# Kernel optimization log

Hardware: AMD Instinct MI355X
Metric: run time of the kernel (lower is better)

## Reference

```python
import jax, jax.numpy as jnp
import numpy as np

B, L, D, F = 1, 4096, 4096, 11008
# (start, end, side): side 0 = vision expert, side 1 = language expert.
# Mirrors merge_section_size over alternating contiguous vision/language token ranges.
SEGMENTS = [(0, 1024, 0), (1024, 2048, 1), (2048, 3072, 0), (3072, 4096, 1)]


def setup_inputs() -> dict:
    key = jax.random.key(0)
    ks = jax.random.split(key, 7)
    s = 0.02  # weight init scale
    hidden_states = jax.random.normal(ks[0], (B, L, D), jnp.float32)
    tt = np.zeros((B, L), np.int32)
    for a, b, side in SEGMENTS:
        tt[:, a:b] = side
    token_type_ids = jnp.asarray(tt)
    lg_w = jax.random.normal(ks[1], (D, F), jnp.float32) * s
    lu_w = jax.random.normal(ks[2], (D, F), jnp.float32) * s
    ld_w = jax.random.normal(ks[3], (F, D), jnp.float32) * s
    vg_w = jax.random.normal(ks[4], (D, F), jnp.float32) * s
    vu_w = jax.random.normal(ks[5], (D, F), jnp.float32) * s
    vd_w = jax.random.normal(ks[6], (F, D), jnp.float32) * s
    return {
        'hidden_states': hidden_states,
        'token_type_ids': token_type_ids,
        'lg_w': lg_w, 'lu_w': lu_w, 'ld_w': ld_w,
        'vg_w': vg_w, 'vu_w': vu_w, 'vd_w': vd_w,
    }


def _swiglu_mlp(x, gw, uw, dw):
    # x: [B, T, D] -> [B, T, D]; down(silu(gate(x)) * up(x))
    h = jax.nn.silu(jnp.einsum('btd,df->btf', x, gw)) * jnp.einsum('btd,df->btf', x, uw)
    return jnp.einsum('btf,fd->btd', h, dw)


def reference(hidden_states, token_type_ids, lg_w, lu_w, ld_w, vg_w, vu_w, vd_w):
    # Split-dispatch over static contiguous segments, then concat along seq dim.
    outs = []
    for a, b, side in SEGMENTS:
        seg = hidden_states[:, a:b, :]
        if side == 1:
            outs.append(_swiglu_mlp(seg, lg_w, lu_w, ld_w))
        else:
            outs.append(_swiglu_mlp(seg, vg_w, vu_w, vd_w))
    return jnp.concatenate(outs, axis=1)
```

## Files before the change

kernel.cpp:

```cpp
#include <hip/hip_runtime.h>
#include <math.h>

typedef unsigned short u16;
typedef short s16x8 __attribute__((ext_vector_type(8)));
typedef float f32x4 __attribute__((ext_vector_type(4)));

#define GLOAD16(gp, lp)                                                        \
  __builtin_amdgcn_global_load_lds(                                            \
      (const __attribute__((address_space(1))) void*)(gp),                     \
      (__attribute__((address_space(3))) void*)(lp), 16, 0, 0)

__device__ __forceinline__ u16 f2bf(float f) {
  union { float f; unsigned u; } v; v.f = f;
  unsigned r = v.u + 0x7fffu + ((v.u >> 16) & 1u);
  return (u16)(r >> 16);
}

__global__ __launch_bounds__(256) void prep_kernel(
    const float* __restrict__ in0, const float* __restrict__ in1,
    const float* __restrict__ in2, const float* __restrict__ in3,
    const float* __restrict__ in4, const float* __restrict__ in5,
    const float* __restrict__ xin,
    u16* __restrict__ o01, u16* __restrict__ o23,
    u16* __restrict__ o4, u16* __restrict__ o5, u16* __restrict__ xout) {
  const int mat = blockIdx.y;
  const int t = threadIdx.x;
  if (mat == 6) {
    if (blockIdx.x >= 8192) return;
    size_t i = ((size_t)blockIdx.x * 256 + t) * 8;
    float4 a = *(const float4*)(xin + i);
    float4 b = *(const float4*)(xin + i + 4);
    s16x8 v;
    v[0] = (short)f2bf(a.x); v[1] = (short)f2bf(a.y);
    v[2] = (short)f2bf(a.z); v[3] = (short)f2bf(a.w);
    v[4] = (short)f2bf(b.x); v[5] = (short)f2bf(b.y);
    v[6] = (short)f2bf(b.z); v[7] = (short)f2bf(b.w);
    *(s16x8*)(xout + i) = v;
    return;
  }
  __shared__ float s[64 * 65];
  const float* in; u16* out;
  switch (mat) {
    case 0: in = in0; out = o01; break;
    case 1: in = in1; out = o01; break;
    case 2: in = in2; out = o23; break;
    case 3: in = in3; out = o23; break;
    case 4: in = in4; out = o4; break;
    default: in = in5; out = o5; break;
  }
  const int R = (mat < 4) ? 4096 : 11008;
  const int C = (mat < 4) ? 11008 : 4096;
  const int nTc = C >> 6;
  const int tr = blockIdx.x / nTc, tc = blockIdx.x - tr * nTc;
  const int r0 = tr << 6, c0 = tc << 6;
#pragma unroll
  for (int p = 0; p < 4; ++p) {
    const int lr = p * 16 + (t >> 4);
    const int lc = (t & 15) * 4;
    float4 v = *(const float4*)(in + (size_t)(r0 + lr) * C + (c0 + lc));
    float* sp = &s[lr * 65 + lc];
    sp[0] = v.x; sp[1] = v.y; sp[2] = v.z; sp[3] = v.w;
  }
  __syncthreads();
#pragma unroll
  for (int q = 0; q < 2; ++q) {
    const int oc = q * 32 + (t >> 3);
    const int orr = (t & 7) * 8;
    s16x8 v;
#pragma unroll
    for (int i = 0; i < 8; ++i) v[i] = (short)f2bf(s[(orr + i) * 65 + oc]);
    const int f = c0 + oc;
    size_t orow;
    if (mat < 4) orow = (size_t)((f >> 4) << 5) + ((mat & 1) << 4) + (f & 15);
    else         orow = (size_t)f;
    *(s16x8*)(out + orow * R + (r0 + orr)) = v;
  }
}

#define SBAR() __builtin_amdgcn_s_barrier()
#define LGKM0() asm volatile("s_waitcnt lgkmcnt(0)")
#define LGKM8() asm volatile("s_waitcnt lgkmcnt(8)")
#define VMCNT6() asm volatile("s_waitcnt vmcnt(6)")
#define VMCNT0() asm volatile("s_waitcnt vmcnt(0)")

__global__ __launch_bounds__(512, 1) void gemm_gateup_persist(
    const u16* __restrict__ A, const u16* __restrict__ Bl,
    const u16* __restrict__ Bv, const int* __restrict__ tt,
    u16* __restrict__ H) {
  __shared__ u16 sA[2][2][128][64];
  __shared__ u16 sB[2][2][128][64];

  const int bid = blockIdx.x;
  const int c = ((bid >> 7) << 3) | (bid & 7);
  const int mT = (bid >> 3) & 15;
  const int ntiles = (c < 6) ? 6 : 5;
  const int FK = ntiles * 64;

  const int t = threadIdx.x;
  const int lane = t & 63;
  const int rlo = lane & 15;
  const int hi = lane >> 4;
  const int wn = (t >> 6) & 3;
  const int wm = (t >> 8) & 1;

  const int side = tt[mT << 8];
  const u16* B = side ? Bl : Bv;

  const int rowq = t >> 3;
  const int gsw = ((t & 7) ^ (rowq & 7)) << 4;
  const char* srcA = (const char*)A + (size_t)(mT * 256 + rowq) * 8192 + gsw;
  const char* srcB0 = (const char*)B + ((size_t)(c * 256) + rowq) * 8192 + gsw;
  char* ldsA = (char*)&sA[0][0][0][0];
  char* ldsB = (char*)&sB[0][0][0][0];
  const int woff = (t & 448) << 4;

#define PSTG_A(d, h, q)                                                        \
  do {                                                                         \
    const char* _pa = srcA + ((q) & 63) * 128;                                 \
    GLOAD16(_pa + (size_t)((h) * 128) * 8192,                                  \
            ldsA + (d) * 32768 + (h) * 16384 + woff);                          \
    GLOAD16(_pa + (size_t)((h) * 128 + 64) * 8192,                             \
            ldsA + (d) * 32768 + (h) * 16384 + 8192 + woff);                   \
  } while (0)
#define PSTG_B(d, h, q)                                                        \
  do {                                                                         \
    const char* _pb = srcB0 + (size_t)((q) >> 6) * 33554432 +                  \
                      (size_t)((h) * 128) * 8192 + ((q) & 63) * 128;           \
    GLOAD16(_pb, ldsB + (d) * 32768 + (h) * 16384 + woff);                     \
    GLOAD16(_pb + (size_t)64 * 8192,                                           \
            ldsB + (d) * 32768 + (h) * 16384 + 8192 + woff);                   \
  } while (0)

  const int cxa = (hi ^ (rlo & 7)) << 4;
  const int cxb = ((4 + hi) ^ (rlo & 7)) << 4;
  const int arow = (wm * 64 + rlo) * 128;
  const int brow = (wn * 32 + rlo) * 128;

  s16x8 af[4][2], bf[2][2][2];
  f32x4 acc[8][4];
  const f32x4 z = {0.f, 0.f, 0.f, 0.f};
#pragma unroll
  for (int i = 0; i < 8; ++i)
#pragma unroll
    for (int j = 0; j < 4; ++j) acc[i][j] = z;

#define LDA(d, mh)                                                             \
  do {                                                                         \
    _Pragma("unroll") for (int fi = 0; fi < 4; ++fi) {                         \
      const char* p = ldsA + (d) * 32768 + (mh) * 16384 + arow + fi * 2048;    \
      af[fi][0] = *(const s16x8*)(p + cxa);                                    \
      af[fi][1] = *(const s16x8*)(p + cxb);                                    \
    }                                                                          \
  } while (0)
#define LDBS(bi, d, nh)                                                        \
  do {                                                                         \
    _Pragma("unroll") for (int gi = 0; gi < 2; ++gi) {                         \
      const char* p = ldsB + (d) * 32768 + (nh) * 16384 + brow + gi * 2048;    \
      bf[bi][gi][0] = *(const s16x8*)(p + cxa);                                \
      bf[bi][gi][1] = *(const s16x8*)(p + cxb);                                \
    }                                                                          \
  } while (0)
#define MFMA16(mh, nh)                                                         \
  do {                                                                         \
    __builtin_amdgcn_s_setprio(1);                                             \
    _Pragma("unroll") for (int fi = 0; fi < 4; ++fi)                           \
        _Pragma("unroll") for (int gi = 0; gi < 2; ++gi) {                     \
      acc[(mh)*4 + fi][(nh)*2 + gi] = __builtin_amdgcn_mfma_f32_16x16x32_bf16( \
          af[fi][0], bf[nh][gi][0], acc[(mh)*4 + fi][(nh)*2 + gi], 0, 0, 0);   \
      acc[(mh)*4 + fi][(nh)*2 + gi] = __builtin_amdgcn_mfma_f32_16x16x32_bf16( \
          af[fi][1], bf[nh][gi][1], acc[(mh)*4 + fi][(nh)*2 + gi], 0, 0, 0);   \
    }                                                                          \
    __builtin_amdgcn_s_setprio(0);                                             \
  } while (0)

#define GU_EPI(nTv)                                                            \
  do {                                                                         \
    const int _nT = (nTv);                                                     \
    _Pragma("unroll") for (int mh = 0; mh < 2; ++mh)                           \
        _Pragma("unroll") for (int fi = 0; fi < 4; ++fi) {                     \
      const int row0 = mT * 256 + mh * 128 + wm * 64 + fi * 16 + hi * 4;       \
      _Pragma("unroll") for (int nh = 0; nh < 2; ++nh) {                       \
        const int fc = _nT * 128 + (nh * 4 + wn) * 16 + rlo;                   \
        const f32x4 g = acc[mh * 4 + fi][nh * 2 + 0];                          \
        const f32x4 u = acc[mh * 4 + fi][nh * 2 + 1];                          \
        _Pragma("unroll") for (int r = 0; r < 4; ++r) {                        \
          const float gv = g[r];                                               \
          const float hv = gv / (1.f + __expf(-gv)) * u[r];                    \
          H[(size_t)(row0 + r) * 11008 + fc] = f2bf(hv);                       \
        }                                                                      \
      }                                                                        \
    }                                                                          \
  } while (0)

  PSTG_A(0, 0, 0); PSTG_B(0, 0, 0); PSTG_B(0, 1, 0); PSTG_A(0, 1, 0);
  PSTG_A(1, 0, 1); PSTG_B(1, 0, 1); PSTG_B(1, 1, 1);
  VMCNT6();
  SBAR();

  for (int T = 0; T < FK - 2; T += 2) {
    LDA(0, 0); LDBS(0, 0, 0);
    PSTG_A(1, 1, T + 1);
    LGKM8();
    SBAR(); LGKM0(); MFMA16(0, 0); SBAR();
    LDBS(1, 0, 1);
    PSTG_A(0, 0, T + 2);
    SBAR(); LGKM0(); MFMA16(0, 1); SBAR();
    LDA(0, 1);
    PSTG_B(0, 0, T + 2);
    SBAR(); LGKM0(); MFMA16(1, 1); SBAR();
    PSTG_B(0, 1, T + 2);
    VMCNT6();
    SBAR(); MFMA16(1, 0); SBAR();
    LDA(1, 0); LDBS(0, 1, 0);
    PSTG_A(0, 1, T + 2);
    LGKM8();
    SBAR(); LGKM0(); MFMA16(0, 0); SBAR();
    LDBS(1, 1, 1);
    PSTG_A(1, 0, T + 3);
    SBAR(); LGKM0(); MFMA16(0, 1); SBAR();
    LDA(1, 1);
    PSTG_B(1, 0, T + 3);
    SBAR(); LGKM0(); MFMA16(1, 1); SBAR();
    PSTG_B(1, 1, T + 3);
    VMCNT6();
    SBAR(); MFMA16(1, 0); SBAR();

    if ((T & 63) == 62) {
      GU_EPI(c + 16 * (T >> 6));
#pragma unroll
      for (int i = 0; i < 8; ++i)
#pragma unroll
        for (int j = 0; j < 4; ++j) acc[i][j] = z;
    }
  }
  {
    LDA(0, 0); LDBS(0, 0, 0);
    PSTG_A(1, 1, FK - 1);
    LGKM8();
    SBAR(); LGKM0(); MFMA16(0, 0); SBAR();
    LDBS(1, 0, 1);
    SBAR(); LGKM0(); MFMA16(0, 1); SBAR();
    LDA(0, 1);
    SBAR(); LGKM0(); MFMA16(1, 1); SBAR();
    VMCNT0();
    SBAR(); MFMA16(1, 0); SBAR();
    LDA(1, 0); LDBS(0, 1, 0);
    LGKM8();
    SBAR(); LGKM0(); MFMA16(0, 0); SBAR();
    LDBS(1, 1, 1);
    SBAR(); LGKM0(); MFMA16(0, 1); SBAR();
    LDA(1, 1);
    SBAR(); LGKM0(); MFMA16(1, 1); SBAR();
    MFMA16(1, 0);
  }
  GU_EPI(c + 16 * (ntiles - 1));
#undef PSTG_A
#undef PSTG_B
#undef LDA
#undef LDBS
#undef MFMA16
#undef GU_EPI
}

__global__ __launch_bounds__(512, 1) void gemm_down(
    const u16* __restrict__ A, const u16* __restrict__ Bl,
    const u16* __restrict__ Bv, const int* __restrict__ tt,
    float* __restrict__ O) {
  constexpr int KB = 22016;
  constexpr int NK = KB / 128;
  __shared__ u16 sA[2][2][128][64];
  __shared__ u16 sB[2][2][128][64];

  const int bid = blockIdx.x;
  const int wg = (bid & 7) * 32 + (bid >> 3);
  const int mT = wg & 15;
  const int nT = wg >> 4;

  const int t = threadIdx.x;
  const int lane = t & 63;
  const int rlo = lane & 15;
  const int hi = lane >> 4;
  const int wn = (t >> 6) & 3;
  const int wm = (t >> 8) & 1;

  const int side = tt[mT << 8];
  const u16* B = side ? Bl : Bv;

  const int rowq = t >> 3;
  const int gsw = ((t & 7) ^ (rowq & 7)) << 4;
  const char* srcA = (const char*)A + (size_t)(mT * 256 + rowq) * KB + gsw;
  const char* srcB = (const char*)B + (size_t)(nT * 256 + rowq) * KB + gsw;
  char* ldsA = (char*)&sA[0][0][0][0];
  char* ldsB = (char*)&sB[0][0][0][0];
  const int woff = (t & 448) << 4;

#define STG_A(d, h, kt)                                                        \
  do {                                                                         \
    GLOAD16(srcA + (size_t)((h) * 128) * KB + (kt) * 128,                      \
            ldsA + (d) * 32768 + (h) * 16384 + woff);                          \
    GLOAD16(srcA + (size_t)((h) * 128 + 64) * KB + (kt) * 128,                 \
            ldsA + (d) * 32768 + (h) * 16384 + 8192 + woff);                   \
  } while (0)
#define STG_B(d, h, kt)                                                        \
  do {                                                                         \
    GLOAD16(srcB + (size_t)((h) * 128) * KB + (kt) * 128,                      \
            ldsB + (d) * 32768 + (h) * 16384 + woff);                          \
    GLOAD16(srcB + (size_t)((h) * 128 + 64) * KB + (kt) * 128,                 \
            ldsB + (d) * 32768 + (h) * 16384 + 8192 + woff);                   \
  } while (0)

  const int cxa = (hi ^ (rlo & 7)) << 4;
  const int cxb = ((4 + hi) ^ (rlo & 7)) << 4;
  const int arow = (wm * 64 + rlo) * 128;
  const int brow = (wn * 32 + rlo) * 128;

  s16x8 af[4][2], bf[2][2][2];
  f32x4 acc[8][4];
  const f32x4 z = {0.f, 0.f, 0.f, 0.f};
#pragma unroll
  for (int i = 0; i < 8; ++i)
#pragma unroll
    for (int j = 0; j < 4; ++j) acc[i][j] = z;

#define LDA(d, mh)                                                             \
  do {                                                                         \
    _Pragma("unroll") for (int fi = 0; fi < 4; ++fi) {                         \
      const char* p = ldsA + (d) * 32768 + (mh) * 16384 + arow + fi * 2048;    \
      af[fi][0] = *(const s16x8*)(p + cxa);                                    \
      af[fi][1] = *(const s16x8*)(p + cxb);                                    \
    }                                                                          \
  } while (0)
#define LDBS(bi, d, nh)                                                        \
  do {                                                                         \
    _Pragma("unroll") for (int gi = 0; gi < 2; ++gi) {                         \
      const char* p = ldsB + (d) * 32768 + (nh) * 16384 + brow + gi * 2048;    \
      bf[bi][gi][0] = *(const s16x8*)(p + cxa);                                \
      bf[bi][gi][1] = *(const s16x8*)(p + cxb);                                \
    }                                                                          \
  } while (0)
#define MFMA16(mh, nh)                                                         \
  do {                                                                         \
    __builtin_amdgcn_s_setprio(1);                                             \
    _Pragma("unroll") for (int fi = 0; fi < 4; ++fi)                           \
        _Pragma("unroll") for (int gi = 0; gi < 2; ++gi) {                     \
      acc[(mh)*4 + fi][(nh)*2 + gi] = __builtin_amdgcn_mfma_f32_16x16x32_bf16( \
          af[fi][0], bf[nh][gi][0], acc[(mh)*4 + fi][(nh)*2 + gi], 0, 0, 0);   \
      acc[(mh)*4 + fi][(nh)*2 + gi] = __builtin_amdgcn_mfma_f32_16x16x32_bf16( \
          af[fi][1], bf[nh][gi][1], acc[(mh)*4 + fi][(nh)*2 + gi], 0, 0, 0);   \
    }                                                                          \
    __builtin_amdgcn_s_setprio(0);                                             \
  } while (0)

  STG_A(0, 0, 0); STG_B(0, 0, 0); STG_B(0, 1, 0); STG_A(0, 1, 0);
  STG_A(1, 0, 1); STG_B(1, 0, 1); STG_B(1, 1, 1);
  VMCNT6();
  SBAR();

  for (int T = 0; T < NK - 2; T += 2) {
    LDA(0, 0); LDBS(0, 0, 0);
    STG_A(1, 1, T + 1);
    LGKM8();
    SBAR(); LGKM0(); MFMA16(0, 0); SBAR();
    LDBS(1, 0, 1);
    STG_A(0, 0, T + 2);
    SBAR(); LGKM0(); MFMA16(0, 1); SBAR();
    LDA(0, 1);
    STG_B(0, 0, T + 2);
    SBAR(); LGKM0(); MFMA16(1, 1); SBAR();
    STG_B(0, 1, T + 2);
    VMCNT6();
    SBAR(); MFMA16(1, 0); SBAR();
    LDA(1, 0); LDBS(0, 1, 0);
    STG_A(0, 1, T + 2);
    LGKM8();
    SBAR(); LGKM0(); MFMA16(0, 0); SBAR();
    LDBS(1, 1, 1);
    STG_A(1, 0, T + 3);
    SBAR(); LGKM0(); MFMA16(0, 1); SBAR();
    LDA(1, 1);
    STG_B(1, 0, T + 3);
    SBAR(); LGKM0(); MFMA16(1, 1); SBAR();
    STG_B(1, 1, T + 3);
    VMCNT6();
    SBAR(); MFMA16(1, 0); SBAR();
  }
  {
    LDA(0, 0); LDBS(0, 0, 0);
    STG_A(1, 1, NK - 1);
    LGKM8();
    SBAR(); LGKM0(); MFMA16(0, 0); SBAR();
    LDBS(1, 0, 1);
    SBAR(); LGKM0(); MFMA16(0, 1); SBAR();
    LDA(0, 1);
    SBAR(); LGKM0(); MFMA16(1, 1); SBAR();
    VMCNT0();
    SBAR(); MFMA16(1, 0); SBAR();
    LDA(1, 0); LDBS(0, 1, 0);
    LGKM8();
    SBAR(); LGKM0(); MFMA16(0, 0); SBAR();
    LDBS(1, 1, 1);
    SBAR(); LGKM0(); MFMA16(0, 1); SBAR();
    LDA(1, 1);
    SBAR(); LGKM0(); MFMA16(1, 1); SBAR();
    MFMA16(1, 0);
  }

#pragma unroll
  for (int mh = 0; mh < 2; ++mh)
#pragma unroll
    for (int fi = 0; fi < 4; ++fi) {
      const int row0 = mT * 256 + mh * 128 + wm * 64 + fi * 16 + hi * 4;
#pragma unroll
      for (int nh = 0; nh < 2; ++nh)
#pragma unroll
        for (int gi = 0; gi < 2; ++gi) {
          const int col = nT * 256 + nh * 128 + wn * 32 + gi * 16 + rlo;
          const f32x4 a = acc[mh * 4 + fi][nh * 2 + gi];
#pragma unroll
          for (int r = 0; r < 4; ++r)
            O[(size_t)(row0 + r) * 4096 + col] = a[r];
        }
    }
#undef STG_A
#undef STG_B
#undef LDA
#undef LDBS
#undef MFMA16
}

extern "C" void kernel_launch(void* const* d_in, const int* in_sizes, int n_in,
                              void* d_out, int out_size, void* d_ws, size_t ws_size,
                              hipStream_t stream) {
  (void)in_sizes; (void)n_in; (void)out_size; (void)ws_size;
  const float* x  = (const float*)d_in[0];
  const int*   tt = (const int*)d_in[1];
  const float* lg = (const float*)d_in[2];
  const float* lu = (const float*)d_in[3];
  const float* ld = (const float*)d_in[4];
  const float* vg = (const float*)d_in[5];
  const float* vu = (const float*)d_in[6];
  const float* vd = (const float*)d_in[7];

  u16* ws  = (u16*)d_ws;
  u16* xbf = ws;
  u16* GUl = xbf + 16777216;
  u16* GUv = GUl + 90177536;
  u16* ldT = GUv + 90177536;
  u16* vdT = ldT + 45088768;
  u16* hbuf = vdT + 45088768;

  prep_kernel<<<dim3(11008, 7), dim3(256), 0, stream>>>(
      lg, lu, vg, vu, ld, vd, x, GUl, GUv, ldT, vdT, xbf);
  gemm_gateup_persist<<<dim3(256), dim3(512), 0, stream>>>(
      xbf, GUl, GUv, tt, hbuf);
  gemm_down<<<dim3(256), dim3(512), 0, stream>>>(hbuf, ldT, vdT, tt, (float*)d_out);
}
```

Baseline: 1.304 ms.

## Replace static persistent tile assignment in gate/up GEMM with atomic work queue

The gate/up GEMM no longer hands each of its 256 persistent blocks a fixed column group of 5 or 6 tiles. Blocks now pull tiles from a global atomic counter (1376 tiles, n-major with 16 M tiles per N tile), and each tile runs its own prologue, main loop, drain and SiLU epilogue. This is meant to even out the load imbalance between blocks doing 6 and 5 tiles. In exchange it adds an atomic, two barriers and a full pipeline refill per tile, and the memset adds a small extra launch.

```diff
diff --git a/kernel.cpp b/kernel.cpp
--- a/kernel.cpp
+++ b/kernel.cpp
@@ -83,18 +83,13 @@
 #define VMCNT6() asm volatile("s_waitcnt vmcnt(6)")
 #define VMCNT0() asm volatile("s_waitcnt vmcnt(0)")
 
-__global__ __launch_bounds__(512, 1) void gemm_gateup_persist(
+__global__ __launch_bounds__(512, 1) void gemm_gateup_queue(
     const u16* __restrict__ A, const u16* __restrict__ Bl,
     const u16* __restrict__ Bv, const int* __restrict__ tt,
-    u16* __restrict__ H) {
+    u16* __restrict__ H, int* __restrict__ qcnt) {
   __shared__ u16 sA[2][2][128][64];
   __shared__ u16 sB[2][2][128][64];
-
-  const int bid = blockIdx.x;
-  const int c = ((bid >> 7) << 3) | (bid & 7);
-  const int mT = (bid >> 3) & 15;
-  const int ntiles = (c < 6) ? 6 : 5;
-  const int FK = ntiles * 64;
+  __shared__ int sQ;
 
   const int t = threadIdx.x;
   const int lane = t & 63;
@@ -103,33 +98,11 @@
   const int wn = (t >> 6) & 3;
   const int wm = (t >> 8) & 1;
 
-  const int side = tt[mT << 8];
-  const u16* B = side ? Bl : Bv;
-
   const int rowq = t >> 3;
   const int gsw = ((t & 7) ^ (rowq & 7)) << 4;
-  const char* srcA = (const char*)A + (size_t)(mT * 256 + rowq) * 8192 + gsw;
-  const char* srcB0 = (const char*)B + ((size_t)(c * 256) + rowq) * 8192 + gsw;
   char* ldsA = (char*)&sA[0][0][0][0];
   char* ldsB = (char*)&sB[0][0][0][0];
   const int woff = (t & 448) << 4;
-
-#define PSTG_A(d, h, q)                                                        \
-  do {                                                                         \
-    const char* _pa = srcA + ((q) & 63) * 128;                                 \
-    GLOAD16(_pa + (size_t)((h) * 128) * 8192,                                  \
-            ldsA + (d) * 32768 + (h) * 16384 + woff);                          \
-    GLOAD16(_pa + (size_t)((h) * 128 + 64) * 8192,                             \
-            ldsA + (d) * 32768 + (h) * 16384 + 8192 + woff);                   \
-  } while (0)
-#define PSTG_B(d, h, q)                                                        \
-  do {                                                                         \
-    const char* _pb = srcB0 + (size_t)((q) >> 6) * 33554432 +                  \
-                      (size_t)((h) * 128) * 8192 + ((q) & 63) * 128;           \
-    GLOAD16(_pb, ldsB + (d) * 32768 + (h) * 16384 + woff);                     \
-    GLOAD16(_pb + (size_t)64 * 8192,                                           \
-            ldsB + (d) * 32768 + (h) * 16384 + 8192 + woff);                   \
-  } while (0)
 
   const int cxa = (hi ^ (rlo & 7)) << 4;
   const int cxb = ((4 + hi) ^ (rlo & 7)) << 4;
@@ -139,11 +112,21 @@
   s16x8 af[4][2], bf[2][2][2];
   f32x4 acc[8][4];
   const f32x4 z = {0.f, 0.f, 0.f, 0.f};
-#pragma unroll
-  for (int i = 0; i < 8; ++i)
-#pragma unroll
-    for (int j = 0; j < 4; ++j) acc[i][j] = z;
-
+
+#define QSTG_A(d, h, kt)                                                       \
+  do {                                                                         \
+    GLOAD16(srcA + (size_t)((h) * 128) * 8192 + (kt) * 128,                    \
+            ldsA + (d) * 32768 + (h) * 16384 + woff);                          \
+    GLOAD16(srcA + (size_t)((h) * 128 + 64) * 8192 + (kt) * 128,               \
+            ldsA + (d) * 32768 + (h) * 16384 + 8192 + woff);                   \
+  } while (0)
+#define QSTG_B(d, h, kt)                                                       \
+  do {                                                                         \
+    GLOAD16(srcB + (size_t)((h) * 128) * 8192 + (kt) * 128,                    \
+            ldsB + (d) * 32768 + (h) * 16384 + woff);                          \
+    GLOAD16(srcB + (size_t)((h) * 128 + 64) * 8192 + (kt) * 128,               \
+            ldsB + (d) * 32768 + (h) * 16384 + 8192 + woff);                   \
+  } while (0)
 #define LDA(d, mh)                                                             \
   do {                                                                         \
     _Pragma("unroll") for (int fi = 0; fi < 4; ++fi) {                         \
@@ -173,93 +156,102 @@
     __builtin_amdgcn_s_setprio(0);                                             \
   } while (0)
 
-#define GU_EPI(nTv)                                                            \
-  do {                                                                         \
-    const int _nT = (nTv);                                                     \
-    _Pragma("unroll") for (int mh = 0; mh < 2; ++mh)                           \
-        _Pragma("unroll") for (int fi = 0; fi < 4; ++fi) {                     \
-      const int row0 = mT * 256 + mh * 128 + wm * 64 + fi * 16 + hi * 4;       \
-      _Pragma("unroll") for (int nh = 0; nh < 2; ++nh) {                       \
-        const int fc = _nT * 128 + (nh * 4 + wn) * 16 + rlo;                   \
-        const f32x4 g = acc[mh * 4 + fi][nh * 2 + 0];                          \
-        const f32x4 u = acc[mh * 4 + fi][nh * 2 + 1];                          \
-        _Pragma("unroll") for (int r = 0; r < 4; ++r) {                        \
-          const float gv = g[r];                                               \
-          const float hv = gv / (1.f + __expf(-gv)) * u[r];                    \
-          H[(size_t)(row0 + r) * 11008 + fc] = f2bf(hv);                       \
-        }                                                                      \
-      }                                                                        \
-    }                                                                          \
-  } while (0)
-
-  PSTG_A(0, 0, 0); PSTG_B(0, 0, 0); PSTG_B(0, 1, 0); PSTG_A(0, 1, 0);
-  PSTG_A(1, 0, 1); PSTG_B(1, 0, 1); PSTG_B(1, 1, 1);
-  VMCNT6();
-  SBAR();
-
-  for (int T = 0; T < FK - 2; T += 2) {
-    LDA(0, 0); LDBS(0, 0, 0);
-    PSTG_A(1, 1, T + 1);
-    LGKM8();
-    SBAR(); LGKM0(); MFMA16(0, 0); SBAR();
-    LDBS(1, 0, 1);
-    PSTG_A(0, 0, T + 2);
-    SBAR(); LGKM0(); MFMA16(0, 1); SBAR();
-    LDA(0, 1);
-    PSTG_B(0, 0, T + 2);
-    SBAR(); LGKM0(); MFMA16(1, 1); SBAR();
-    PSTG_B(0, 1, T + 2);
+  for (;;) {
+    __syncthreads();
+    if (t == 0) sQ = atomicAdd(qcnt, 1);
+    __syncthreads();
+    const int q = sQ;
+    if (q >= 1376) break;
+    const int nT = q >> 4;
+    const int mT = q & 15;
+    const int side = tt[mT << 8];
+    const u16* GU = side ? Bl : Bv;
+    const char* srcA = (const char*)A + (size_t)(mT * 256 + rowq) * 8192 + gsw;
+    const char* srcB = (const char*)GU + (size_t)(nT * 256 + rowq) * 8192 + gsw;
+
+#pragma unroll
+    for (int i = 0; i < 8; ++i)
+#pragma unroll
+      for (int j = 0; j < 4; ++j) acc[i][j] = z;
+
+    QSTG_A(0, 0, 0); QSTG_B(0, 0, 0); QSTG_B(0, 1, 0); QSTG_A(0, 1, 0);
+    QSTG_A(1, 0, 1); QSTG_B(1, 0, 1); QSTG_B(1, 1, 1);
     VMCNT6();
-    SBAR(); MFMA16(1, 0); SBAR();
-    LDA(1, 0); LDBS(0, 1, 0);
-    PSTG_A(0, 1, T + 2);
-    LGKM8();
-    SBAR(); LGKM0(); MFMA16(0, 0); SBAR();
-    LDBS(1, 1, 1);
-    PSTG_A(1, 0, T + 3);
-    SBAR(); LGKM0(); MFMA16(0, 1); SBAR();
-    LDA(1, 1);
-    PSTG_B(1, 0, T + 3);
-    SBAR(); LGKM0(); MFMA16(1, 1); SBAR();
-    PSTG_B(1, 1, T + 3);
-    VMCNT6();
-    SBAR(); MFMA16(1, 0); SBAR();
-
-    if ((T & 63) == 62) {
-      GU_EPI(c + 16 * (T >> 6));
-#pragma unroll
-      for (int i = 0; i < 8; ++i)
-#pragma unroll
-        for (int j = 0; j < 4; ++j) acc[i][j] = z;
+    SBAR();
+
+    for (int T = 0; T < 62; T += 2) {
+      LDA(0, 0); LDBS(0, 0, 0);
+      QSTG_A(1, 1, T + 1);
+      LGKM8();
+      SBAR(); LGKM0(); MFMA16(0, 0); SBAR();
+      LDBS(1, 0, 1);
+      QSTG_A(0, 0, T + 2);
+      SBAR(); LGKM0(); MFMA16(0, 1); SBAR();
+      LDA(0, 1);
+      QSTG_B(0, 0, T + 2);
+      SBAR(); LGKM0(); MFMA16(1, 1); SBAR();
+      QSTG_B(0, 1, T + 2);
+      VMCNT6();
+      SBAR(); MFMA16(1, 0); SBAR();
+      LDA(1, 0); LDBS(0, 1, 0);
+      QSTG_A(0, 1, T + 2);
+      LGKM8();
+      SBAR(); LGKM0(); MFMA16(0, 0); SBAR();
+      LDBS(1, 1, 1);
+      QSTG_A(1, 0, T + 3);
+      SBAR(); LGKM0(); MFMA16(0, 1); SBAR();
+      LDA(1, 1);
+      QSTG_B(1, 0, T + 3);
+      SBAR(); LGKM0(); MFMA16(1, 1); SBAR();
+      QSTG_B(1, 1, T + 3);
+      VMCNT6();
+      SBAR(); MFMA16(1, 0); SBAR();
     }
-  }
-  {
-    LDA(0, 0); LDBS(0, 0, 0);
-    PSTG_A(1, 1, FK - 1);
-    LGKM8();
-    SBAR(); LGKM0(); MFMA16(0, 0); SBAR();
-    LDBS(1, 0, 1);
-    SBAR(); LGKM0(); MFMA16(0, 1); SBAR();
-    LDA(0, 1);
-    SBAR(); LGKM0(); MFMA16(1, 1); SBAR();
-    VMCNT0();
-    SBAR(); MFMA16(1, 0); SBAR();
-    LDA(1, 0); LDBS(0, 1, 0);
-    LGKM8();
-    SBAR(); LGKM0(); MFMA16(0, 0); SBAR();
-    LDBS(1, 1, 1);
-    SBAR(); LGKM0(); MFMA16(0, 1); SBAR();
-    LDA(1, 1);
-    SBAR(); LGKM0(); MFMA16(1, 1); SBAR();
-    MFMA16(1, 0);
-  }
-  GU_EPI(c + 16 * (ntiles - 1));
-#undef PSTG_A
-#undef PSTG_B
+    {
+      LDA(0, 0); LDBS(0, 0, 0);
+      QSTG_A(1, 1, 63);
+      LGKM8();
+      SBAR(); LGKM0(); MFMA16(0, 0); SBAR();
+      LDBS(1, 0, 1);
+      SBAR(); LGKM0(); MFMA16(0, 1); SBAR();
+      LDA(0, 1);
+      SBAR(); LGKM0(); MFMA16(1, 1); SBAR();
+      VMCNT0();
+      SBAR(); MFMA16(1, 0); SBAR();
+      LDA(1, 0); LDBS(0, 1, 0);
+      LGKM8();
+      SBAR(); LGKM0(); MFMA16(0, 0); SBAR();
+      LDBS(1, 1, 1);
+      SBAR(); LGKM0(); MFMA16(0, 1); SBAR();
+      LDA(1, 1);
+      SBAR(); LGKM0(); MFMA16(1, 1); SBAR();
+      MFMA16(1, 0);
+    }
+
+#pragma unroll
+    for (int mh = 0; mh < 2; ++mh)
+#pragma unroll
+      for (int fi = 0; fi < 4; ++fi) {
+        const int row0 = mT * 256 + mh * 128 + wm * 64 + fi * 16 + hi * 4;
+#pragma unroll
+        for (int nh = 0; nh < 2; ++nh) {
+          const int fc = nT * 128 + (nh * 4 + wn) * 16 + rlo;
+          const f32x4 g = acc[mh * 4 + fi][nh * 2 + 0];
+          const f32x4 u = acc[mh * 4 + fi][nh * 2 + 1];
+#pragma unroll
+          for (int r = 0; r < 4; ++r) {
+            const float gv = g[r];
+            const float hv = gv / (1.f + __expf(-gv)) * u[r];
+            H[(size_t)(row0 + r) * 11008 + fc] = f2bf(hv);
+          }
+        }
+      }
+  }
+#undef QSTG_A
+#undef QSTG_B
 #undef LDA
 #undef LDBS
 #undef MFMA16
-#undef GU_EPI
 }
 
 __global__ __launch_bounds__(512, 1) void gemm_down(
@@ -448,10 +440,12 @@
   u16* ldT = GUv + 90177536;
   u16* vdT = ldT + 45088768;
   u16* hbuf = vdT + 45088768;
-
+  int* qcnt = (int*)(hbuf + 45088768);
+
+  hipMemsetAsync(qcnt, 0, 4, stream);
   prep_kernel<<<dim3(11008, 7), dim3(256), 0, stream>>>(
       lg, lu, vg, vu, ld, vd, x, GUl, GUv, ldT, vdT, xbf);
-  gemm_gateup_persist<<<dim3(256), dim3(512), 0, stream>>>(
-      xbf, GUl, GUv, tt, hbuf);
+  gemm_gateup_queue<<<dim3(256), dim3(512), 0, stream>>>(
+      xbf, GUl, GUv, tt, hbuf, qcnt);
   gemm_down<<<dim3(256), dim3(512), 0, stream>>>(hbuf, ldT, vdT, tt, (float*)d_out);
 }
```

Result: no change. 1.314 ms (+0.7%).

## Triple-buffer B tiles in gate/up GEMM to prefetch one step further ahead

Applied to the files above, without the earlier changes.

Grows the B shared-memory staging in the persistent gate/up GEMM from two to three buffers. The B tiles for each k-step are now issued one iteration earlier, and the buffer offsets rotate at runtime. The loop tail is peeled into two drain blocks to match. The aim is to hide more global-load latency on the weight operand. In exchange, LDS use reaches the full per-CU capacity, buffer addressing becomes dynamic, and the vmcnt wait counts may no longer match the deeper in-flight load queue.

```diff
diff --git a/kernel.cpp b/kernel.cpp
--- a/kernel.cpp
+++ b/kernel.cpp
@@ -88,7 +88,7 @@
     const u16* __restrict__ Bv, const int* __restrict__ tt,
     u16* __restrict__ H) {
   __shared__ u16 sA[2][2][128][64];
-  __shared__ u16 sB[2][2][128][64];
+  __shared__ u16 sB[3][2][128][64];
 
   const int bid = blockIdx.x;
   const int c = ((bid >> 7) << 3) | (bid & 7);
@@ -122,13 +122,13 @@
     GLOAD16(_pa + (size_t)((h) * 128 + 64) * 8192,                             \
             ldsA + (d) * 32768 + (h) * 16384 + 8192 + woff);                   \
   } while (0)
-#define PSTG_B(d, h, q)                                                        \
+#define PSTG_B(boffB, h, q)                                                    \
   do {                                                                         \
     const char* _pb = srcB0 + (size_t)((q) >> 6) * 33554432 +                  \
                       (size_t)((h) * 128) * 8192 + ((q) & 63) * 128;           \
-    GLOAD16(_pb, ldsB + (d) * 32768 + (h) * 16384 + woff);                     \
+    GLOAD16(_pb, ldsB + (boffB) + (h) * 16384 + woff);                         \
     GLOAD16(_pb + (size_t)64 * 8192,                                           \
-            ldsB + (d) * 32768 + (h) * 16384 + 8192 + woff);                   \
+            ldsB + (boffB) + (h) * 16384 + 8192 + woff);                       \
   } while (0)
 
   const int cxa = (hi ^ (rlo & 7)) << 4;
@@ -152,10 +152,10 @@
       af[fi][1] = *(const s16x8*)(p + cxb);                                    \
     }                                                                          \
   } while (0)
-#define LDBS(bi, d, nh)                                                        \
+#define LDBS(bi, boffB, nh)                                                    \
   do {                                                                         \
     _Pragma("unroll") for (int gi = 0; gi < 2; ++gi) {                         \
-      const char* p = ldsB + (d) * 32768 + (nh) * 16384 + brow + gi * 2048;    \
+      const char* p = ldsB + (boffB) + (nh) * 16384 + brow + gi * 2048;        \
       bf[bi][gi][0] = *(const s16x8*)(p + cxa);                                \
       bf[bi][gi][1] = *(const s16x8*)(p + cxb);                                \
     }                                                                          \
@@ -193,35 +193,37 @@
   } while (0)
 
   PSTG_A(0, 0, 0); PSTG_B(0, 0, 0); PSTG_B(0, 1, 0); PSTG_A(0, 1, 0);
-  PSTG_A(1, 0, 1); PSTG_B(1, 0, 1); PSTG_B(1, 1, 1);
+  PSTG_A(1, 0, 1); PSTG_B(32768, 0, 1); PSTG_B(32768, 1, 1);
+  PSTG_B(65536, 0, 2); PSTG_B(65536, 1, 2);
   VMCNT6();
   SBAR();
 
-  for (int T = 0; T < FK - 2; T += 2) {
-    LDA(0, 0); LDBS(0, 0, 0);
+  int bB0 = 0, bB1 = 32768, bB2 = 65536;
+  for (int T = 0; T < FK - 4; T += 2) {
+    LDA(0, 0); LDBS(0, bB0, 0);
     PSTG_A(1, 1, T + 1);
     LGKM8();
     SBAR(); LGKM0(); MFMA16(0, 0); SBAR();
-    LDBS(1, 0, 1);
+    LDBS(1, bB0, 1);
     PSTG_A(0, 0, T + 2);
     SBAR(); LGKM0(); MFMA16(0, 1); SBAR();
     LDA(0, 1);
-    PSTG_B(0, 0, T + 2);
-    SBAR(); LGKM0(); MFMA16(1, 1); SBAR();
-    PSTG_B(0, 1, T + 2);
+    PSTG_B(bB0, 0, T + 3);
+    SBAR(); LGKM0(); MFMA16(1, 1); SBAR();
+    PSTG_B(bB0, 1, T + 3);
     VMCNT6();
     SBAR(); MFMA16(1, 0); SBAR();
-    LDA(1, 0); LDBS(0, 1, 0);
+    LDA(1, 0); LDBS(0, bB1, 0);
     PSTG_A(0, 1, T + 2);
     LGKM8();
     SBAR(); LGKM0(); MFMA16(0, 0); SBAR();
-    LDBS(1, 1, 1);
+    LDBS(1, bB1, 1);
     PSTG_A(1, 0, T + 3);
     SBAR(); LGKM0(); MFMA16(0, 1); SBAR();
     LDA(1, 1);
-    PSTG_B(1, 0, T + 3);
-    SBAR(); LGKM0(); MFMA16(1, 1); SBAR();
-    PSTG_B(1, 1, T + 3);
+    PSTG_B(bB1, 0, T + 4);
+    SBAR(); LGKM0(); MFMA16(1, 1); SBAR();
+    PSTG_B(bB1, 1, T + 4);
     VMCNT6();
     SBAR(); MFMA16(1, 0); SBAR();
 
@@ -232,26 +234,50 @@
 #pragma unroll
         for (int j = 0; j < 4; ++j) acc[i][j] = z;
     }
+    const int btmp = bB2; bB2 = bB1; bB1 = bB0; bB0 = btmp;
   }
   {
-    LDA(0, 0); LDBS(0, 0, 0);
-    PSTG_A(1, 1, FK - 1);
-    LGKM8();
-    SBAR(); LGKM0(); MFMA16(0, 0); SBAR();
-    LDBS(1, 0, 1);
+    const int T = FK - 4;
+    LDA(0, 0); LDBS(0, bB0, 0);
+    PSTG_A(1, 1, T + 1);
+    LGKM8();
+    SBAR(); LGKM0(); MFMA16(0, 0); SBAR();
+    LDBS(1, bB0, 1);
+    PSTG_A(0, 0, T + 2);
     SBAR(); LGKM0(); MFMA16(0, 1); SBAR();
     LDA(0, 1);
-    SBAR(); LGKM0(); MFMA16(1, 1); SBAR();
+    PSTG_B(bB0, 0, T + 3);
+    SBAR(); LGKM0(); MFMA16(1, 1); SBAR();
+    PSTG_B(bB0, 1, T + 3);
+    VMCNT6();
+    SBAR(); MFMA16(1, 0); SBAR();
+    LDA(1, 0); LDBS(0, bB1, 0);
+    PSTG_A(0, 1, T + 2);
+    LGKM8();
+    SBAR(); LGKM0(); MFMA16(0, 0); SBAR();
+    LDBS(1, bB1, 1);
+    PSTG_A(1, 0, T + 3);
+    SBAR(); LGKM0(); MFMA16(0, 1); SBAR();
+    LDA(1, 1);
+    SBAR(); LGKM0(); MFMA16(1, 1); SBAR();
+    PSTG_A(1, 1, T + 3);
     VMCNT0();
     SBAR(); MFMA16(1, 0); SBAR();
-    LDA(1, 0); LDBS(0, 1, 0);
-    LGKM8();
-    SBAR(); LGKM0(); MFMA16(0, 0); SBAR();
-    LDBS(1, 1, 1);
-    SBAR(); LGKM0(); MFMA16(0, 1); SBAR();
+    const int btmp = bB2; bB2 = bB1; bB1 = bB0; bB0 = btmp;
+  }
+  {
+    LDA(0, 0); LDBS(0, bB0, 0);
+    LGKM0(); MFMA16(0, 0);
+    LDBS(1, bB0, 1);
+    LGKM0(); MFMA16(0, 1);
+    LDA(0, 1);
+    LGKM0(); MFMA16(1, 1); MFMA16(1, 0);
+    LDA(1, 0); LDBS(0, bB1, 0);
+    LGKM0(); MFMA16(0, 0);
+    LDBS(1, bB1, 1);
+    LGKM0(); MFMA16(0, 1);
     LDA(1, 1);
-    SBAR(); LGKM0(); MFMA16(1, 1); SBAR();
-    MFMA16(1, 0);
+    LGKM0(); MFMA16(1, 1); MFMA16(1, 0);
   }
   GU_EPI(c + 16 * (ntiles - 1));
 #undef PSTG_A
```

New measurement: 1.369 ms. 1.05x slower.
